# Performance work log

Hardware: AMD Instinct MI355X
Metric: run time of the kernel (lower is better)

The kernel has to match this reference:

```python
import jax, jax.numpy as jnp
import numpy as np

N = 100000        # nodes
E = 1600000       # edges (avg degree 16)
F_IN = 128        # num_node_features
H = 64            # hidden_channels
F_EDGE = 8        # num_edge_features (output dim per edge)


def setup_inputs() -> dict:
    key = jax.random.key(0)
    ks = jax.random.split(key, 9)
    x = jax.random.normal(ks[0], (N, F_IN), dtype=jnp.float32)
    edge_index = jax.random.randint(ks[1], (2, E), 0, N, dtype=jnp.int32)
    s = 0.05
    W1 = jax.random.normal(ks[2], (F_IN, H), jnp.float32) * s
    b1 = jnp.zeros((H,), jnp.float32)
    W2 = jax.random.normal(ks[3], (H, H), jnp.float32) * s
    b2 = jnp.zeros((H,), jnp.float32)
    Wl = jax.random.normal(ks[4], (2 * H, F_EDGE), jnp.float32) * s
    bl = jnp.zeros((F_EDGE,), jnp.float32)
    return {"x": x, "edge_index": edge_index,
            "W1": W1, "b1": b1, "W2": W2, "b2": b2, "Wl": Wl, "bl": bl}


def gcn_conv(x, W, b, row, col, n):
    # GCNConv: h = D^{-1/2} (A + I) D^{-1/2} (x W) + b
    h = x @ W
    sl = jnp.arange(n, dtype=row.dtype)          # self-loops
    r = jnp.concatenate([row, sl])
    c = jnp.concatenate([col, sl])
    ones = jnp.ones(r.shape[0], dtype=h.dtype)
    deg = jax.ops.segment_sum(ones, c, num_segments=n)      # in-degree incl. self-loop
    dinv = jax.lax.rsqrt(jnp.maximum(deg, 1e-12))
    norm = dinv[r] * dinv[c]                                 # symmetric normalization
    agg = jax.ops.segment_sum(norm[:, None] * h[r], c, num_segments=n)
    return agg + b


def reference(x, edge_index, W1, b1, W2, b2, Wl, bl):
    row, col = edge_index[0], edge_index[1]
    h = jax.nn.relu(gcn_conv(x, W1, b1, row, col, N))
    # dropout p=0.5 is identity at inference (training=False)
    h = jax.nn.relu(gcn_conv(h, W2, b2, row, col, N))
    x_i = h[row]                                  # [E, H]
    x_j = h[col]                                  # [E, H]
    return jnp.concatenate([x_i, x_j], axis=-1) @ Wl + bl   # [E, F_EDGE]
```

## Files before the change

### kernel.cpp

```cpp
#include <hip/hip_runtime.h>
#include <hip/hip_bf16.h>

static constexpr int NN  = 100000;
static constexpr int NE  = 1600000;
static constexpr int FIN = 128;
static constexpr int HD  = 64;

static constexpr int NB    = 256;
static constexpr int NPB   = 392;
static constexpr int EPB   = NE / NB;
static constexpr unsigned long long DIV392_MAGIC = 43826197ULL;

typedef __attribute__((ext_vector_type(8))) short bf16x8;
typedef __attribute__((ext_vector_type(4))) float f32x4;

__device__ __forceinline__ float bf2f(unsigned short u) {
    return __uint_as_float(((unsigned int)u) << 16);
}
__device__ __forceinline__ unsigned short f2bf(float f) {
    __hip_bfloat16 hb = __float2bfloat16(f);
    return *(unsigned short*)&hb;
}
__device__ __forceinline__ int bucket_of(int c) {
    return (int)(((unsigned long long)(unsigned int)c * DIV392_MAGIC) >> 34);
}

__global__ __launch_bounds__(256) void k_detect(const unsigned short* __restrict__ xu,
                                                int* __restrict__ flag) {
    __shared__ int sd[256];
    int t = threadIdx.x;
    int cnt = 0;
    for (int k = t; k < 4096; k += 256) {
        unsigned short u = xu[2 * k];
        int ex = (u >> 7) & 0xFF;
        cnt += (ex >= 110 && ex <= 135) ? 1 : 0;
    }
    sd[t] = cnt;
    __syncthreads();
    for (int off = 128; off > 0; off >>= 1) {
        if (t < off) sd[t] += sd[t + off];
        __syncthreads();
    }
    if (t == 0) flag[0] = (sd[0] >= 2048) ? 1 : 0;
}

__device__ __forceinline__ float load_in(const void* p, size_t i, int isbf) {
    return isbf ? bf2f(((const unsigned short*)p)[i]) : ((const float*)p)[i];
}

__global__ __launch_bounds__(256) void k_hist(const int* __restrict__ col, int* __restrict__ hist) {
    __shared__ int h[NB];
    int t = threadIdx.x;
    h[t] = 0;
    __syncthreads();
    int base = blockIdx.x * EPB;
    for (int e = base + t; e < base + EPB; e += 256)
        atomicAdd(&h[bucket_of(col[e])], 1);
    __syncthreads();
    hist[t * NB + blockIdx.x] = h[t];
}

__global__ __launch_bounds__(256) void k_gscan1(int* __restrict__ a, int* __restrict__ bsums) {
    __shared__ int sd[256];
    int t = threadIdx.x;
    int base = blockIdx.x * 1024 + t * 4;
    int v0 = a[base], v1 = a[base + 1], v2 = a[base + 2], v3 = a[base + 3];
    int tsum = v0 + v1 + v2 + v3;
    sd[t] = tsum;
    __syncthreads();
    for (int off = 1; off < 256; off <<= 1) {
        int tmp = (t >= off) ? sd[t - off] : 0;
        __syncthreads();
        sd[t] += tmp;
        __syncthreads();
    }
    int run = sd[t] - tsum;
    a[base] = run; run += v0;
    a[base + 1] = run; run += v1;
    a[base + 2] = run; run += v2;
    a[base + 3] = run;
    if (t == 255) bsums[blockIdx.x] = sd[t];
}

__global__ __launch_bounds__(256) void k_gscan2(int* __restrict__ bsums) {
    __shared__ int sd[256];
    int t = threadIdx.x;
    int v = (t < 64) ? bsums[t] : 0;
    sd[t] = v;
    __syncthreads();
    for (int off = 1; off < 256; off <<= 1) {
        int tmp = (t >= off) ? sd[t - off] : 0;
        __syncthreads();
        sd[t] += tmp;
        __syncthreads();
    }
    if (t < 64) bsums[t] = sd[t] - v;
}

__global__ __launch_bounds__(256) void k_gscan3(int* __restrict__ a, const int* __restrict__ bsums) {
    int t = threadIdx.x;
    int base = blockIdx.x * 1024 + t * 4;
    int add = bsums[blockIdx.x];
    a[base] += add; a[base + 1] += add; a[base + 2] += add; a[base + 3] += add;
}

__global__ __launch_bounds__(256) void k_binfill(const int* __restrict__ row, const int* __restrict__ col,
                                                 const int* __restrict__ histS, int2* __restrict__ csr_tmp) {
    __shared__ int cur[NB];
    int t = threadIdx.x;
    cur[t] = histS[t * NB + blockIdx.x];
    __syncthreads();
    int base = blockIdx.x * EPB;
    for (int e = base + t; e < base + EPB; e += 256) {
        int r = row[e], c = col[e];
        int p = atomicAdd(&cur[bucket_of(c)], 1);
        csr_tmp[p] = make_int2(r, c);
    }
}

__global__ __launch_bounds__(256) void k_bsort(const int2* __restrict__ csr_tmp,
                                               const int* __restrict__ histS,
                                               int* __restrict__ csr_src,
                                               int* __restrict__ start,
                                               float* __restrict__ dinv) {
    __shared__ int cnt[512];
    __shared__ int cur[512];
    int t = threadIdx.x;
    int k = blockIdx.x;
    int S = histS[k * NB];
    int E = (k < NB - 1) ? histS[(k + 1) * NB] : NE;
    int nbase = k * NPB;
    cnt[t] = 0; cnt[t + 256] = 0;
    __syncthreads();
    for (int e = S + t; e < E; e += 256)
        atomicAdd(&cnt[csr_tmp[e].y - nbase], 1);
    __syncthreads();
    int rc0 = cnt[t], rc1 = cnt[t + 256];
    for (int d = 1; d < 512; d <<= 1) {
        int idx = (t + 1) * (d << 1) - 1;
        if (idx < 512) cnt[idx] += cnt[idx - d];
        __syncthreads();
    }
    if (t == 0) cnt[511] = 0;
    __syncthreads();
    for (int d = 256; d >= 1; d >>= 1) {
        int idx = (t + 1) * (d << 1) - 1;
        if (idx < 512) { int tmp = cnt[idx - d]; cnt[idx - d] = cnt[idx]; cnt[idx] += tmp; }
        __syncthreads();
    }
    int n0 = nbase + t;
    if (n0 < NN) {
        start[n0] = S + cnt[t] + rc0;
        dinv[n0] = rsqrtf((float)(rc0 + 1));
    }
    int li = t + 256;
    int n1 = nbase + li;
    if (li < NPB && n1 < NN) {
        start[n1] = S + cnt[li] + rc1;
        dinv[n1] = rsqrtf((float)(rc1 + 1));
    }
    cur[t] = cnt[t]; cur[t + 256] = cnt[t + 256];
    __syncthreads();
    for (int e = S + t; e < E; e += 256) {
        int2 rc = csr_tmp[e];
        int p = atomicAdd(&cur[rc.y - nbase], 1);
        csr_src[S + p] = rc.x;
    }
}

template <int K, bool XDUAL>
__global__ __launch_bounds__(256) void k_gemm_mfma(const void* __restrict__ X,
                                                   const void* __restrict__ W,
                                                   const float* __restrict__ dinv,
                                                   __hip_bfloat16* __restrict__ Y,
                                                   const int* __restrict__ flag) {
    constexpr int KT = K / 32;
    __shared__ unsigned short Bs[KT * 4 * 64 * 8];
    int isbf = flag[0];
    for (int tup = threadIdx.x; tup < KT * 4 * 64; tup += 256) {
        int l  = tup & 63;
        int nt = (tup >> 6) & 3;
        int kt = tup >> 8;
        int n  = nt * 16 + (l & 15);
        int kb = kt * 32 + (l >> 4) * 8;
        unsigned short tmp[8];
#pragma unroll
        for (int j = 0; j < 8; ++j) tmp[j] = f2bf(load_in(W, (size_t)(kb + j) * HD + n, isbf));
        *((uint4*)&Bs[(size_t)tup * 8]) = *((const uint4*)tmp);
    }
    __syncthreads();
    int wave = threadIdx.x >> 6, lane = threadIdx.x & 63;
    int quad = lane >> 4, m = lane & 15;
    int row0 = blockIdx.x * 64 + wave * 16;
    int row  = row0 + m;
    int rowc = (row < NN) ? row : (NN - 1);
    bool xf32 = XDUAL && (isbf == 0);
    const char* xrow = (const char*)X + (size_t)rowc * K * (xf32 ? 4 : 2);
    f32x4 acc[4];
#pragma unroll
    for (int nt = 0; nt < 4; ++nt) acc[nt] = (f32x4){0.f, 0.f, 0.f, 0.f};
#pragma unroll
    for (int kt = 0; kt < KT; ++kt) {
        bf16x8 a;
        if (!xf32) {
            a = *((const bf16x8*)(xrow + (size_t)(kt * 32 + quad * 8) * 2));
        } else {
            const float4* fp = (const float4*)(xrow + (size_t)(kt * 32 + quad * 8) * 4);
            float4 u0 = fp[0], u1 = fp[1];
            unsigned short tmp[8] = {f2bf(u0.x), f2bf(u0.y), f2bf(u0.z), f2bf(u0.w),
                                     f2bf(u1.x), f2bf(u1.y), f2bf(u1.z), f2bf(u1.w)};
            a = *((const bf16x8*)tmp);
        }
#pragma unroll
        for (int nt = 0; nt < 4; ++nt) {
            bf16x8 b = *((const bf16x8*)&Bs[(size_t)((kt * 4 + nt) * 64 + lane) * 8]);
            acc[nt] = __builtin_amdgcn_mfma_f32_16x16x32_bf16(a, b, acc[nt], 0, 0, 0);
        }
    }
#pragma unroll
    for (int r = 0; r < 4; ++r) {
        int orow = row0 + quad * 4 + r;
        if (orow < NN) {
            float sc = dinv[orow];
#pragma unroll
            for (int nt = 0; nt < 4; ++nt)
                Y[(size_t)orow * HD + nt * 16 + m] = __float2bfloat16(acc[nt][r] * sc);
        }
    }
}

__global__ __launch_bounds__(256) void k_agg_relu(const unsigned short* __restrict__ T,
                                                  unsigned short* __restrict__ Hout,
                                                  const int* __restrict__ endOff,
                                                  const int* __restrict__ csr_src,
                                                  const float* __restrict__ dinv,
                                                  const void* __restrict__ bias,
                                                  const int* __restrict__ flag) {
    int isbf = flag[0];
    int lane = threadIdx.x & 63, wave = threadIdx.x >> 6;
    int q  = lane >> 4;
    int fl = (lane & 15) * 4;
    int i = blockIdx.x * 16 + wave * 4 + q;
    int end = endOff[i];
    int beg = (i == 0) ? 0 : endOff[i - 1];
    float a0, a1, a2, a3;
    {
        ushort4 t = *((const ushort4*)(T + (size_t)i * HD + fl));
        a0 = bf2f(t.x); a1 = bf2f(t.y); a2 = bf2f(t.z); a3 = bf2f(t.w);
    }
    int k = beg;
    for (; k + 3 < end; k += 4) {
        int s0 = csr_src[k], s1 = csr_src[k + 1], s2 = csr_src[k + 2], s3 = csr_src[k + 3];
        ushort4 t0 = *((const ushort4*)(T + (size_t)s0 * HD + fl));
        ushort4 t1 = *((const ushort4*)(T + (size_t)s1 * HD + fl));
        ushort4 t2 = *((const ushort4*)(T + (size_t)s2 * HD + fl));
        ushort4 t3 = *((const ushort4*)(T + (size_t)s3 * HD + fl));
        a0 += bf2f(t0.x) + bf2f(t1.x) + bf2f(t2.x) + bf2f(t3.x);
        a1 += bf2f(t0.y) + bf2f(t1.y) + bf2f(t2.y) + bf2f(t3.y);
        a2 += bf2f(t0.z) + bf2f(t1.z) + bf2f(t2.z) + bf2f(t3.z);
        a3 += bf2f(t0.w) + bf2f(t1.w) + bf2f(t2.w) + bf2f(t3.w);
    }
    for (; k < end; ++k) {
        int s = csr_src[k];
        ushort4 t = *((const ushort4*)(T + (size_t)s * HD + fl));
        a0 += bf2f(t.x); a1 += bf2f(t.y); a2 += bf2f(t.z); a3 += bf2f(t.w);
    }
    float di = dinv[i];
    float b0 = load_in(bias, fl + 0, isbf), b1 = load_in(bias, fl + 1, isbf);
    float b2 = load_in(bias, fl + 2, isbf), b3 = load_in(bias, fl + 3, isbf);
    ushort4 o;
    o.x = f2bf(fmaxf(fmaf(di, a0, b0), 0.f));
    o.y = f2bf(fmaxf(fmaf(di, a1, b1), 0.f));
    o.z = f2bf(fmaxf(fmaf(di, a2, b2), 0.f));
    o.w = f2bf(fmaxf(fmaf(di, a3, b3), 0.f));
    *((ushort4*)(Hout + (size_t)i * HD + fl)) = o;
}

__global__ __launch_bounds__(256) void k_pgemm(const __hip_bfloat16* __restrict__ H,
                                               const void* __restrict__ Wl,
                                               const void* __restrict__ bl,
                                               float* __restrict__ P,
                                               const int* __restrict__ flag) {
    int isbf = flag[0];
    int wave = threadIdx.x >> 6, lane = threadIdx.x & 63;
    int quad = lane >> 4, m = lane & 15;
    bf16x8 bfr[2];
#pragma unroll
    for (int kt = 0; kt < 2; ++kt) {
        unsigned short tmp[8];
#pragma unroll
        for (int j = 0; j < 8; ++j) {
            int kk = kt * 32 + quad * 8 + j;
            float w = (m < 8) ? load_in(Wl, (size_t)kk * 8 + m, isbf)
                              : load_in(Wl, (size_t)(64 + kk) * 8 + (m - 8), isbf);
            tmp[j] = f2bf(w);
        }
        bfr[kt] = *((const bf16x8*)tmp);
    }
    float binit = (m < 8) ? load_in(bl, m, isbf) : 0.f;
    int row0 = blockIdx.x * 64 + wave * 16;
    int row  = row0 + m;
    int rowc = (row < NN) ? row : (NN - 1);
    const __hip_bfloat16* hrow = H + (size_t)rowc * HD;
    bf16x8 x0 = *((const bf16x8*)(hrow + quad * 8));
    bf16x8 x1 = *((const bf16x8*)(hrow + 32 + quad * 8));
    f32x4 acc = (f32x4){binit, binit, binit, binit};
    acc = __builtin_amdgcn_mfma_f32_16x16x32_bf16(x0, bfr[0], acc, 0, 0, 0);
    acc = __builtin_amdgcn_mfma_f32_16x16x32_bf16(x1, bfr[1], acc, 0, 0, 0);
#pragma unroll
    for (int r = 0; r < 4; ++r) {
        int orow = row0 + quad * 4 + r;
        if (orow < NN) P[(size_t)orow * 16 + m] = acc[r];
    }
}

__global__ __launch_bounds__(256) void k_edge_add(const float* __restrict__ P,
                                                  const int* __restrict__ erow,
                                                  const int* __restrict__ ecol,
                                                  void* __restrict__ out,
                                                  const int* __restrict__ flag) {
    int isbf = flag[0];
    int e = blockIdx.x * 256 + threadIdx.x;
    int i = erow[e], j = ecol[e];
    const float4* Pi = (const float4*)(P + (size_t)i * 16);
    const float4* Pj = (const float4*)(P + (size_t)j * 16);
    float4 a0 = Pi[0], a1 = Pi[1];
    float4 c0 = Pj[2], c1 = Pj[3];
    float v[8] = {a0.x + c0.x, a0.y + c0.y, a0.z + c0.z, a0.w + c0.w,
                  a1.x + c1.x, a1.y + c1.y, a1.z + c1.z, a1.w + c1.w};
    if (isbf) {
        union { unsigned short h[8]; uint4 u; } p;
#pragma unroll
        for (int o = 0; o < 8; ++o) p.h[o] = f2bf(v[o]);
        *((uint4*)((__hip_bfloat16*)out + (size_t)e * 8)) = p.u;
    } else {
        float* op = (float*)out + (size_t)e * 8;
        ((float4*)op)[0] = make_float4(v[0], v[1], v[2], v[3]);
        ((float4*)op)[1] = make_float4(v[4], v[5], v[6], v[7]);
    }
}

extern "C" void kernel_launch(void* const* d_in, const int* in_sizes, int n_in,
                              void* d_out, int out_size, void* d_ws, size_t ws_size,
                              hipStream_t stream) {
    const void* x  = d_in[0];
    const int*  ei = (const int*)d_in[1];
    const void* W1 = d_in[2];
    const void* b1 = d_in[3];
    const void* W2 = d_in[4];
    const void* b2 = d_in[5];
    const void* Wl = d_in[6];
    const void* bl = d_in[7];
    const int* row = ei;
    const int* col = ei + NE;

    char* ws = (char*)d_ws;
    int*   flag    = (int*)ws;    ws += 16;
    int*   hist    = (int*)ws;    ws += (size_t)NB * NB * 4;
    int*   bsums   = (int*)ws;    ws += 256 * 4;
    int*   start   = (int*)ws;    ws += (size_t)NN * 4;
    float* dinv    = (float*)ws;  ws += (size_t)NN * 4;
    int2*  csr_tmp = (int2*)ws;   ws += (size_t)NE * 8;
    int*   csr_src = (int*)ws;    ws += (size_t)NE * 4;
    __hip_bfloat16* bufT = (__hip_bfloat16*)ws;  ws += (size_t)NN * HD * 2;
    __hip_bfloat16* bufH = (__hip_bfloat16*)ws;  ws += (size_t)NN * HD * 2;
    float* P = (float*)ws;

    int gE   = (NE + 255) / 256;
    int gN16 = NN / 16;
    int gN64 = (NN + 63) / 64;

    k_detect<<<1, 256, 0, stream>>>((const unsigned short*)x, flag);
    k_hist   <<<NB, 256, 0, stream>>>(col, hist);
    k_gscan1 <<<64, 256, 0, stream>>>(hist, bsums);
    k_gscan2 <<<1, 256, 0, stream>>>(bsums);
    k_gscan3 <<<64, 256, 0, stream>>>(hist, bsums);
    k_binfill<<<NB, 256, 0, stream>>>(row, col, hist, csr_tmp);
    k_bsort  <<<NB, 256, 0, stream>>>(csr_tmp, hist, csr_src, start, dinv);

    k_gemm_mfma<FIN, true><<<gN64, 256, 0, stream>>>(x, W1, dinv, bufT, flag);
    k_agg_relu<<<gN16, 256, 0, stream>>>((const unsigned short*)bufT, (unsigned short*)bufH,
                                         start, csr_src, dinv, b1, flag);

    k_gemm_mfma<HD, false><<<gN64, 256, 0, stream>>>(bufH, W2, dinv, bufT, flag);
    k_agg_relu<<<gN16, 256, 0, stream>>>((const unsigned short*)bufT, (unsigned short*)bufH,
                                         start, csr_src, dinv, b2, flag);

    k_pgemm<<<gN64, 256, 0, stream>>>(bufH, Wl, bl, P, flag);
    k_edge_add<<<gE, 256, 0, stream>>>(P, row, col, d_out, flag);
}
```

Baseline: 336.4 us.

## Split feature halves for aggregation, pack CSR temp, bf16 edge table

Several changes are bundled. The transformed features are split into two 32-column halves so each aggregation pass gathers from a smaller table that fits cache better, at the cost of running the aggregation twice. The CSR temp entries are packed into a single int holding the source and local column. k_gscan3 is removed by adding the block sums on the fly. The histogram is privatised per wave, and the per-node edge projection table is stored in bf16, which halves gather traffic but adds rounding error.

```diff
diff --git a/kernel.cpp b/kernel.cpp
--- a/kernel.cpp
+++ b/kernel.cpp
@@ -49,15 +49,16 @@
 }
 
 __global__ __launch_bounds__(256) void k_hist(const int* __restrict__ col, int* __restrict__ hist) {
-    __shared__ int h[NB];
-    int t = threadIdx.x;
-    h[t] = 0;
+    __shared__ int h[4][NB];
+    int t = threadIdx.x, w = t >> 6;
+#pragma unroll
+    for (int r = 0; r < 4; ++r) h[r][t] = 0;
     __syncthreads();
     int base = blockIdx.x * EPB;
     for (int e = base + t; e < base + EPB; e += 256)
-        atomicAdd(&h[bucket_of(col[e])], 1);
-    __syncthreads();
-    hist[t * NB + blockIdx.x] = h[t];
+        atomicAdd(&h[w][bucket_of(col[e])], 1);
+    __syncthreads();
+    hist[t * NB + blockIdx.x] = h[0][t] + h[1][t] + h[2][t] + h[3][t];
 }
 
 __global__ __launch_bounds__(256) void k_gscan1(int* __restrict__ a, int* __restrict__ bsums) {
@@ -97,29 +98,25 @@
     if (t < 64) bsums[t] = sd[t] - v;
 }
 
-__global__ __launch_bounds__(256) void k_gscan3(int* __restrict__ a, const int* __restrict__ bsums) {
-    int t = threadIdx.x;
-    int base = blockIdx.x * 1024 + t * 4;
-    int add = bsums[blockIdx.x];
-    a[base] += add; a[base + 1] += add; a[base + 2] += add; a[base + 3] += add;
-}
-
 __global__ __launch_bounds__(256) void k_binfill(const int* __restrict__ row, const int* __restrict__ col,
-                                                 const int* __restrict__ histS, int2* __restrict__ csr_tmp) {
+                                                 const int* __restrict__ histS, const int* __restrict__ bsums,
+                                                 int* __restrict__ csr_tmp) {
     __shared__ int cur[NB];
     int t = threadIdx.x;
-    cur[t] = histS[t * NB + blockIdx.x];
+    cur[t] = histS[t * NB + blockIdx.x] + bsums[t >> 2];
     __syncthreads();
     int base = blockIdx.x * EPB;
     for (int e = base + t; e < base + EPB; e += 256) {
         int r = row[e], c = col[e];
-        int p = atomicAdd(&cur[bucket_of(c)], 1);
-        csr_tmp[p] = make_int2(r, c);
-    }
-}
-
-__global__ __launch_bounds__(256) void k_bsort(const int2* __restrict__ csr_tmp,
+        int b = bucket_of(c);
+        int p = atomicAdd(&cur[b], 1);
+        csr_tmp[p] = r | ((c - b * NPB) << 17);
+    }
+}
+
+__global__ __launch_bounds__(256) void k_bsort(const int* __restrict__ csr_tmp,
                                                const int* __restrict__ histS,
+                                               const int* __restrict__ bsums,
                                                int* __restrict__ csr_src,
                                                int* __restrict__ start,
                                                float* __restrict__ dinv) {
@@ -127,13 +124,13 @@
     __shared__ int cur[512];
     int t = threadIdx.x;
     int k = blockIdx.x;
-    int S = histS[k * NB];
-    int E = (k < NB - 1) ? histS[(k + 1) * NB] : NE;
+    int S = histS[k * NB] + bsums[k >> 2];
+    int E = (k < NB - 1) ? (histS[(k + 1) * NB] + bsums[(k + 1) >> 2]) : NE;
     int nbase = k * NPB;
     cnt[t] = 0; cnt[t + 256] = 0;
     __syncthreads();
     for (int e = S + t; e < E; e += 256)
-        atomicAdd(&cnt[csr_tmp[e].y - nbase], 1);
+        atomicAdd(&cnt[csr_tmp[e] >> 17], 1);
     __syncthreads();
     int rc0 = cnt[t], rc1 = cnt[t + 256];
     for (int d = 1; d < 512; d <<= 1) {
@@ -162,9 +159,9 @@
     cur[t] = cnt[t]; cur[t + 256] = cnt[t + 256];
     __syncthreads();
     for (int e = S + t; e < E; e += 256) {
-        int2 rc = csr_tmp[e];
-        int p = atomicAdd(&cur[rc.y - nbase], 1);
-        csr_src[S + p] = rc.x;
+        int u = csr_tmp[e];
+        int p = atomicAdd(&cur[u >> 17], 1);
+        csr_src[S + p] = u & 0x1FFFF;
     }
 }
 
@@ -172,7 +169,8 @@
 __global__ __launch_bounds__(256) void k_gemm_mfma(const void* __restrict__ X,
                                                    const void* __restrict__ W,
                                                    const float* __restrict__ dinv,
-                                                   __hip_bfloat16* __restrict__ Y,
+                                                   unsigned short* __restrict__ T0,
+                                                   unsigned short* __restrict__ T1,
                                                    const int* __restrict__ flag) {
     constexpr int KT = K / 32;
     __shared__ unsigned short Bs[KT * 4 * 64 * 8];
@@ -223,38 +221,41 @@
         if (orow < NN) {
             float sc = dinv[orow];
 #pragma unroll
-            for (int nt = 0; nt < 4; ++nt)
-                Y[(size_t)orow * HD + nt * 16 + m] = __float2bfloat16(acc[nt][r] * sc);
+            for (int nt = 0; nt < 4; ++nt) {
+                unsigned short* Th = (nt >= 2) ? T1 : T0;
+                Th[(size_t)orow * 32 + (nt & 1) * 16 + m] = f2bf(acc[nt][r] * sc);
+            }
         }
     }
 }
 
-__global__ __launch_bounds__(256) void k_agg_relu(const unsigned short* __restrict__ T,
+__global__ __launch_bounds__(256) void k_agg_half(const unsigned short* __restrict__ Th,
                                                   unsigned short* __restrict__ Hout,
                                                   const int* __restrict__ endOff,
                                                   const int* __restrict__ csr_src,
                                                   const float* __restrict__ dinv,
                                                   const void* __restrict__ bias,
-                                                  const int* __restrict__ flag) {
+                                                  const int* __restrict__ flag,
+                                                  int half) {
     int isbf = flag[0];
     int lane = threadIdx.x & 63, wave = threadIdx.x >> 6;
-    int q  = lane >> 4;
-    int fl = (lane & 15) * 4;
-    int i = blockIdx.x * 16 + wave * 4 + q;
+    int g  = lane >> 3;
+    int fl = (lane & 7) * 4;
+    int i = blockIdx.x * 32 + wave * 8 + g;
     int end = endOff[i];
     int beg = (i == 0) ? 0 : endOff[i - 1];
     float a0, a1, a2, a3;
     {
-        ushort4 t = *((const ushort4*)(T + (size_t)i * HD + fl));
+        ushort4 t = *((const ushort4*)(Th + (size_t)i * 32 + fl));
         a0 = bf2f(t.x); a1 = bf2f(t.y); a2 = bf2f(t.z); a3 = bf2f(t.w);
     }
     int k = beg;
     for (; k + 3 < end; k += 4) {
         int s0 = csr_src[k], s1 = csr_src[k + 1], s2 = csr_src[k + 2], s3 = csr_src[k + 3];
-        ushort4 t0 = *((const ushort4*)(T + (size_t)s0 * HD + fl));
-        ushort4 t1 = *((const ushort4*)(T + (size_t)s1 * HD + fl));
-        ushort4 t2 = *((const ushort4*)(T + (size_t)s2 * HD + fl));
-        ushort4 t3 = *((const ushort4*)(T + (size_t)s3 * HD + fl));
+        ushort4 t0 = *((const ushort4*)(Th + (size_t)s0 * 32 + fl));
+        ushort4 t1 = *((const ushort4*)(Th + (size_t)s1 * 32 + fl));
+        ushort4 t2 = *((const ushort4*)(Th + (size_t)s2 * 32 + fl));
+        ushort4 t3 = *((const ushort4*)(Th + (size_t)s3 * 32 + fl));
         a0 += bf2f(t0.x) + bf2f(t1.x) + bf2f(t2.x) + bf2f(t3.x);
         a1 += bf2f(t0.y) + bf2f(t1.y) + bf2f(t2.y) + bf2f(t3.y);
         a2 += bf2f(t0.z) + bf2f(t1.z) + bf2f(t2.z) + bf2f(t3.z);
@@ -262,24 +263,25 @@
     }
     for (; k < end; ++k) {
         int s = csr_src[k];
-        ushort4 t = *((const ushort4*)(T + (size_t)s * HD + fl));
+        ushort4 t = *((const ushort4*)(Th + (size_t)s * 32 + fl));
         a0 += bf2f(t.x); a1 += bf2f(t.y); a2 += bf2f(t.z); a3 += bf2f(t.w);
     }
     float di = dinv[i];
-    float b0 = load_in(bias, fl + 0, isbf), b1 = load_in(bias, fl + 1, isbf);
-    float b2 = load_in(bias, fl + 2, isbf), b3 = load_in(bias, fl + 3, isbf);
+    int fg = half * 32 + fl;
+    float b0 = load_in(bias, fg + 0, isbf), b1 = load_in(bias, fg + 1, isbf);
+    float b2 = load_in(bias, fg + 2, isbf), b3 = load_in(bias, fg + 3, isbf);
     ushort4 o;
     o.x = f2bf(fmaxf(fmaf(di, a0, b0), 0.f));
     o.y = f2bf(fmaxf(fmaf(di, a1, b1), 0.f));
     o.z = f2bf(fmaxf(fmaf(di, a2, b2), 0.f));
     o.w = f2bf(fmaxf(fmaf(di, a3, b3), 0.f));
-    *((ushort4*)(Hout + (size_t)i * HD + fl)) = o;
+    *((ushort4*)(Hout + (size_t)i * HD + fg)) = o;
 }
 
 __global__ __launch_bounds__(256) void k_pgemm(const __hip_bfloat16* __restrict__ H,
                                                const void* __restrict__ Wl,
                                                const void* __restrict__ bl,
-                                               float* __restrict__ P,
+                                               unsigned short* __restrict__ P,
                                                const int* __restrict__ flag) {
     int isbf = flag[0];
     int wave = threadIdx.x >> 6, lane = threadIdx.x & 63;
@@ -310,11 +312,11 @@
 #pragma unroll
     for (int r = 0; r < 4; ++r) {
         int orow = row0 + quad * 4 + r;
-        if (orow < NN) P[(size_t)orow * 16 + m] = acc[r];
-    }
-}
-
-__global__ __launch_bounds__(256) void k_edge_add(const float* __restrict__ P,
+        if (orow < NN) P[(size_t)orow * 16 + m] = f2bf(acc[r]);
+    }
+}
+
+__global__ __launch_bounds__(256) void k_edge_add(const unsigned short* __restrict__ P,
                                                   const int* __restrict__ erow,
                                                   const int* __restrict__ ecol,
                                                   void* __restrict__ out,
@@ -322,12 +324,14 @@
     int isbf = flag[0];
     int e = blockIdx.x * 256 + threadIdx.x;
     int i = erow[e], j = ecol[e];
-    const float4* Pi = (const float4*)(P + (size_t)i * 16);
-    const float4* Pj = (const float4*)(P + (size_t)j * 16);
-    float4 a0 = Pi[0], a1 = Pi[1];
-    float4 c0 = Pj[2], c1 = Pj[3];
-    float v[8] = {a0.x + c0.x, a0.y + c0.y, a0.z + c0.z, a0.w + c0.w,
-                  a1.x + c1.x, a1.y + c1.y, a1.z + c1.z, a1.w + c1.w};
+    ushort4 r0 = *((const ushort4*)(P + (size_t)i * 16));
+    ushort4 r1 = *((const ushort4*)(P + (size_t)i * 16 + 4));
+    ushort4 c0 = *((const ushort4*)(P + (size_t)j * 16 + 8));
+    ushort4 c1 = *((const ushort4*)(P + (size_t)j * 16 + 12));
+    float v[8] = {bf2f(r0.x) + bf2f(c0.x), bf2f(r0.y) + bf2f(c0.y),
+                  bf2f(r0.z) + bf2f(c0.z), bf2f(r0.w) + bf2f(c0.w),
+                  bf2f(r1.x) + bf2f(c1.x), bf2f(r1.y) + bf2f(c1.y),
+                  bf2f(r1.z) + bf2f(c1.z), bf2f(r1.w) + bf2f(c1.w)};
     if (isbf) {
         union { unsigned short h[8]; uint4 u; } p;
 #pragma unroll
@@ -360,31 +364,31 @@
     int*   bsums   = (int*)ws;    ws += 256 * 4;
     int*   start   = (int*)ws;    ws += (size_t)NN * 4;
     float* dinv    = (float*)ws;  ws += (size_t)NN * 4;
-    int2*  csr_tmp = (int2*)ws;   ws += (size_t)NE * 8;
+    int*   csr_tmp = (int*)ws;    ws += (size_t)NE * 4;
     int*   csr_src = (int*)ws;    ws += (size_t)NE * 4;
-    __hip_bfloat16* bufT = (__hip_bfloat16*)ws;  ws += (size_t)NN * HD * 2;
+    unsigned short* T0 = (unsigned short*)ws;  ws += (size_t)NN * 32 * 2;
+    unsigned short* T1 = (unsigned short*)ws;  ws += (size_t)NN * 32 * 2;
     __hip_bfloat16* bufH = (__hip_bfloat16*)ws;  ws += (size_t)NN * HD * 2;
-    float* P = (float*)ws;
+    unsigned short* P = (unsigned short*)ws;
 
     int gE   = (NE + 255) / 256;
-    int gN16 = NN / 16;
+    int gN32 = NN / 32;
     int gN64 = (NN + 63) / 64;
 
     k_detect<<<1, 256, 0, stream>>>((const unsigned short*)x, flag);
     k_hist   <<<NB, 256, 0, stream>>>(col, hist);
     k_gscan1 <<<64, 256, 0, stream>>>(hist, bsums);
     k_gscan2 <<<1, 256, 0, stream>>>(bsums);
-    k_gscan3 <<<64, 256, 0, stream>>>(hist, bsums);
-    k_binfill<<<NB, 256, 0, stream>>>(row, col, hist, csr_tmp);
-    k_bsort  <<<NB, 256, 0, stream>>>(csr_tmp, hist, csr_src, start, dinv);
-
-    k_gemm_mfma<FIN, true><<<gN64, 256, 0, stream>>>(x, W1, dinv, bufT, flag);
-    k_agg_relu<<<gN16, 256, 0, stream>>>((const unsigned short*)bufT, (unsigned short*)bufH,
-                                         start, csr_src, dinv, b1, flag);
-
-    k_gemm_mfma<HD, false><<<gN64, 256, 0, stream>>>(bufH, W2, dinv, bufT, flag);
-    k_agg_relu<<<gN16, 256, 0, stream>>>((const unsigned short*)bufT, (unsigned short*)bufH,
-                                         start, csr_src, dinv, b2, flag);
+    k_binfill<<<NB, 256, 0, stream>>>(row, col, hist, bsums, csr_tmp);
+    k_bsort  <<<NB, 256, 0, stream>>>(csr_tmp, hist, bsums, csr_src, start, dinv);
+
+    k_gemm_mfma<FIN, true><<<gN64, 256, 0, stream>>>(x, W1, dinv, T0, T1, flag);
+    k_agg_half<<<gN32, 256, 0, stream>>>(T0, (unsigned short*)bufH, start, csr_src, dinv, b1, flag, 0);
+    k_agg_half<<<gN32, 256, 0, stream>>>(T1, (unsigned short*)bufH, start, csr_src, dinv, b1, flag, 1);
+
+    k_gemm_mfma<HD, false><<<gN64, 256, 0, stream>>>(bufH, W2, dinv, T0, T1, flag);
+    k_agg_half<<<gN32, 256, 0, stream>>>(T0, (unsigned short*)bufH, start, csr_src, dinv, b2, flag, 0);
+    k_agg_half<<<gN32, 256, 0, stream>>>(T1, (unsigned short*)bufH, start, csr_src, dinv, b2, flag, 1);
 
     k_pgemm<<<gN64, 256, 0, stream>>>(bufH, Wl, bl, P, flag);
     k_edge_add<<<gE, 256, 0, stream>>>(P, row, col, d_out, flag);
```

After: 328.9 us. 2.2% less time.
